# Kernel optimization log

Hardware: AMD Instinct MI355X
Metric: run time of the kernel (lower is better)

Reference implementation:

```python
import jax, jax.numpy as jnp
import numpy as np

D_MODEL = 256
NHEAD = 8
HEAD_DIM = D_MODEL // NHEAD
NUM_BOND_TYPES = 5
SCALE = float(np.sqrt(HEAD_DIM))


def setup_inputs() -> dict:
    key = jax.random.key(0)
    ks = jax.random.split(key, 12)
    B, N = 8, 1024
    s = 1.0 / np.sqrt(D_MODEL)
    x = jax.random.normal(ks[0], (B, N, D_MODEL), dtype=jnp.float32)
    adj_matrix = jax.random.randint(ks[1], (B, N, N), 0, NUM_BOND_TYPES, dtype=jnp.int32)
    Wq = jax.random.uniform(ks[2], (D_MODEL, D_MODEL), jnp.float32, -s, s)
    bq = jax.random.uniform(ks[3], (D_MODEL,), jnp.float32, -s, s)
    Wk = jax.random.uniform(ks[4], (D_MODEL, D_MODEL), jnp.float32, -s, s)
    bk = jax.random.uniform(ks[5], (D_MODEL,), jnp.float32, -s, s)
    Wv = jax.random.uniform(ks[6], (D_MODEL, D_MODEL), jnp.float32, -s, s)
    bv = jax.random.uniform(ks[7], (D_MODEL,), jnp.float32, -s, s)
    Wo = jax.random.uniform(ks[8], (D_MODEL, D_MODEL), jnp.float32, -s, s)
    bo = jax.random.uniform(ks[9], (D_MODEL,), jnp.float32, -s, s)
    # edge bias table (num_bond_types, nhead); torch init is zeros, use small randn so it matters
    edge_emb = 0.02 * jax.random.normal(ks[10], (NUM_BOND_TYPES, NHEAD), dtype=jnp.float32)
    return {"x": x, "adj_matrix": adj_matrix, "Wq": Wq, "bq": bq, "Wk": Wk, "bk": bk,
            "Wv": Wv, "bv": bv, "Wo": Wo, "bo": bo, "edge_emb": edge_emb}


def reference(x, adj_matrix, Wq, bq, Wk, bk, Wv, bv, Wo, bo, edge_emb):
    B, N, _ = x.shape
    # projections -> (B, H, N, Dh)
    def proj(W, b):
        return (x @ W.T + b).reshape(B, N, NHEAD, HEAD_DIM).transpose(0, 2, 1, 3)
    Q = proj(Wq, bq)
    K = proj(Wk, bk)
    V = proj(Wv, bv)
    scores = jnp.einsum('bhqd,bhkd->bhqk', Q, K) / SCALE  # (B,H,N,N)
    bias = edge_emb[adj_matrix]                            # (B,N,N,H)
    scores = scores + bias.transpose(0, 3, 1, 2)
    attn = jax.nn.softmax(scores, axis=-1)                 # dropout p=0 (eval) -> identity
    out = jnp.einsum('bhqk,bhkd->bhqd', attn, V)
    out = out.transpose(0, 2, 1, 3).reshape(B, N, D_MODEL)
    return out @ Wo.T + bo
```

## Files before the change

### kernel.cpp

```cpp
#include <hip/hip_runtime.h>
#include <hip/hip_bf16.h>

typedef float f32x4 __attribute__((ext_vector_type(4)));
typedef float f32x16 __attribute__((ext_vector_type(16)));
typedef __bf16 bf16x8 __attribute__((ext_vector_type(8)));
typedef unsigned int uint2v __attribute__((ext_vector_type(2)));

#define MFMA16(a, b, c) __builtin_amdgcn_mfma_f32_16x16x32_bf16((a), (b), (c), 0, 0, 0)
#define MFMA32(a, b, c) __builtin_amdgcn_mfma_f32_32x32x16_bf16((a), (b), (c), 0, 0, 0)

static __device__ __forceinline__ short f2s(float f) {
    __hip_bfloat16 h = __float2bfloat16(f);
    return *reinterpret_cast<short*>(&h);
}
static __device__ __forceinline__ unsigned int cvtpk(float lo, float hi) {
    unsigned int r;
    asm("v_cvt_pk_bf16_f32 %0, %1, %2" : "=v"(r) : "v"(lo), "v"(hi));
    return r;
}
static __device__ __forceinline__ float exp2f_fast(float x) {
#if __has_builtin(__builtin_amdgcn_exp2f)
    return __builtin_amdgcn_exp2f(x);
#else
    return exp2f(x);
#endif
}

__global__ __launch_bounds__(256)
void qkv3_and_gather(const float* __restrict__ x,
                     const float* __restrict__ Wq, const float* __restrict__ bq,
                     const float* __restrict__ Wk, const float* __restrict__ bk,
                     const float* __restrict__ Wv, const float* __restrict__ bv,
                     short* __restrict__ Qb, short* __restrict__ Kb, short* __restrict__ Vb,
                     const int* __restrict__ adj, unsigned int* __restrict__ adjG)
{
    __shared__ short As[128 * 72];
    __shared__ short Bs[3][64 * 72];

    const int bx = blockIdx.x;
    const int tid = threadIdx.x;

    if (bx < 256) {
        const int lane = tid & 63;
        const int wid = tid >> 6;
        const int wr = wid >> 1, wc = wid & 1;
        const int g = lane >> 4, li = lane & 15;

        const int m0 = (bx & 63) * 128;
        const int wc0 = (bx >> 6) * 64;

        const float* Wm[3]  = { Wq, Wk, Wv };
        const float* bm[3]  = { bq, bk, bv };
        short*       Om[3]  = { Qb, Kb, Vb };

        f32x4 acc[3][4][2] = {};

        const int sr = tid >> 4;
        const int sc4 = (tid & 15) * 4;

        for (int k0 = 0; k0 < 256; k0 += 64) {
            __syncthreads();
#pragma unroll
            for (int it = 0; it < 8; ++it) {
                int row = sr + it * 16;
                float4 v = *reinterpret_cast<const float4*>(&x[(m0 + row) * 256 + k0 + sc4]);
                short4 s4;
                s4.x = f2s(v.x); s4.y = f2s(v.y); s4.z = f2s(v.z); s4.w = f2s(v.w);
                *reinterpret_cast<short4*>(&As[row * 72 + sc4]) = s4;
            }
#pragma unroll
            for (int mat = 0; mat < 3; ++mat) {
#pragma unroll
                for (int it = 0; it < 4; ++it) {
                    int row = sr + it * 16;
                    float4 v = *reinterpret_cast<const float4*>(
                        &Wm[mat][(wc0 + row) * 256 + k0 + sc4]);
                    short4 s4;
                    s4.x = f2s(v.x); s4.y = f2s(v.y); s4.z = f2s(v.z); s4.w = f2s(v.w);
                    *reinterpret_cast<short4*>(&Bs[mat][row * 72 + sc4]) = s4;
                }
            }
            __syncthreads();
#pragma unroll
            for (int ks = 0; ks < 2; ++ks) {
                const int kb = ks * 32 + g * 8;
                bf16x8 a[4];
#pragma unroll
                for (int i = 0; i < 4; ++i)
                    a[i] = *reinterpret_cast<const bf16x8*>(&As[(wr * 64 + i * 16 + li) * 72 + kb]);
#pragma unroll
                for (int mat = 0; mat < 3; ++mat) {
                    bf16x8 bfr[2];
#pragma unroll
                    for (int j = 0; j < 2; ++j)
                        bfr[j] = *reinterpret_cast<const bf16x8*>(
                            &Bs[mat][(wc * 32 + j * 16 + li) * 72 + kb]);
#pragma unroll
                    for (int i = 0; i < 4; ++i)
#pragma unroll
                        for (int j = 0; j < 2; ++j)
                            acc[mat][i][j] = MFMA16(a[i], bfr[j], acc[mat][i][j]);
                }
            }
        }

#pragma unroll
        for (int mat = 0; mat < 3; ++mat) {
#pragma unroll
            for (int j = 0; j < 2; ++j) {
                const int colW = wc0 + wc * 32 + j * 16 + li;
                const int h = colW >> 5, d = colW & 31;
                const float bv_ = bm[mat][colW];
#pragma unroll
                for (int i = 0; i < 4; ++i) {
#pragma unroll
                    for (int r = 0; r < 4; ++r) {
                        const int row = m0 + wr * 64 + i * 16 + g * 4 + r;
                        const int bb = row >> 10, nq = row & 1023;
                        Om[mat][((bb * 8 + h) * 1024 + nq) * 32 + d] =
                            f2s(acc[mat][i][j][r] + bv_);
                    }
                }
            }
        }
    } else {
        const int gx = bx - 256;
        const int qt = gx & 31;
        const int b  = (gx >> 5) & 7;
        const int j0 = (gx >> 8) * 8;

        const int4* base = reinterpret_cast<const int4*>(
            adj + ((size_t)(b * 1024 + qt * 32)) * 1024);
        unsigned int* outT = adjG + ((size_t)(b * 32 + qt)) * 16 * 512;

        const int t = tid >> 4;
        const int i = (tid >> 1) & 7;
        const int laneb = 32 * (tid & 1);

#pragma unroll
        for (int jj = 0; jj < 8; ++jj) {
            const int j = j0 + jj;
            const int4 c = base[j * 256 + tid];
            const unsigned int packed =
                (unsigned)c.x | ((unsigned)c.y << 8) | ((unsigned)c.z << 16) | ((unsigned)c.w << 24);
            outT[t * 512 + i * 64 + (j + laneb)] = packed;
        }
    }
}

__global__ __launch_bounds__(256, 4)
void attn12(const short* __restrict__ Qb, const short* __restrict__ Kb,
            const short* __restrict__ Vb, const unsigned int* __restrict__ adjG,
            const float* __restrict__ edge_emb, short* __restrict__ AO)
{
    __shared__ __align__(16) short Ks[4][64 * 36];
    __shared__ __align__(16) short Vt[4][32 * 72];
    __shared__ float Etab[8];

    const int tid = threadIdx.x, lane = tid & 63, wid = tid >> 6;
    const int l5 = lane & 31, h32 = lane >> 5;
    const int qw = wid & 1, kh = wid >> 1;

    const int orig = blockIdx.x + blockIdx.y * 16;
    const int flat = (orig & 7) * 128 + (orig >> 3);
    const int qb = flat & 15, bh = flat >> 4;
    const int b = bh >> 3, h = bh & 7;
    const int qt = qb * 2 + qw;
    const int q  = qt * 32 + l5;

    const short* Qh = Qb + bh * (1024 * 32);
    const short* Kh = Kb + bh * (1024 * 32);
    const short* Vh = Vb + bh * (1024 * 32);
    const unsigned int* adjT = adjG + ((size_t)(b * 32 + qt)) * 16 * 512;

    if (tid < 5) Etab[tid] = __expf(edge_emb[tid * 8 + h]);

    const bf16x8 qf0 = *reinterpret_cast<const bf16x8*>(&Qh[q * 32 + h32 * 8]);
    const bf16x8 qf1 = *reinterpret_cast<const bf16x8*>(&Qh[q * 32 + 16 + h32 * 8]);

    const float c1 = 0.25503486f;
    const f32x16 zero16 = {};

    f32x16 o = {};
    float lr = 0.f;

    const int sr = tid >> 2;
    const int sc = (tid & 3) * 8;
    const int srh = sr >> 3, srl = sr & 7;
    const int scg2 = (sc >> 3) << 1;

#pragma unroll
    for (int u = 0; u < 2; ++u) {
        const int row = u * 512 + sr;
        int4 kr = *reinterpret_cast<const int4*>(&Kh[row * 32 + sc]);
        int4 vr = *reinterpret_cast<const int4*>(&Vh[row * 32 + sc]);
        short* kd = &Ks[u][sr * 36 + sc];
        *reinterpret_cast<short4*>(kd)     = *reinterpret_cast<short4*>(&kr);
        *reinterpret_cast<short4*>(kd + 4) = *(reinterpret_cast<short4*>(&kr) + 1);
        const short* vs = reinterpret_cast<const short*>(&vr);
#pragma unroll
        for (int i = 0; i < 8; ++i) {
            const int swz = srh ^ i ^ scg2;
            Vt[u][(sc + i) * 72 + swz * 8 + srl] = vs[i];
        }
    }
    __syncthreads();

    for (int t = 0; t < 8; ++t) {
        const int cur = (t & 1) * 2;
        const int tt = kh * 8 + t;

        unsigned int a4[8];
#pragma unroll
        for (int i = 0; i < 8; ++i)
            a4[i] = adjT[tt * 512 + i * 64 + lane];

        int4 kn[2], vn[2];
        if (t < 7) {
#pragma unroll
            for (int u = 0; u < 2; ++u) {
                const int row = u * 512 + (t + 1) * 64 + sr;
                kn[u] = *reinterpret_cast<const int4*>(&Kh[row * 32 + sc]);
                vn[u] = *reinterpret_cast<const int4*>(&Vh[row * 32 + sc]);
            }
        }

        f32x16 s[2];
        {
            const short* KsC = &Ks[cur + kh][0];
#pragma unroll
            for (int ks = 0; ks < 2; ++ks) {
                union { short4 h4[2]; bf16x8 v; } kfa, kfb;
                const int rowb = (ks * 32 + l5) * 36;
                kfa.h4[0] = *reinterpret_cast<const short4*>(&KsC[rowb + h32 * 8]);
                kfa.h4[1] = *reinterpret_cast<const short4*>(&KsC[rowb + h32 * 8 + 4]);
                kfb.h4[0] = *reinterpret_cast<const short4*>(&KsC[rowb + 16 + h32 * 8]);
                kfb.h4[1] = *reinterpret_cast<const short4*>(&KsC[rowb + 16 + h32 * 8 + 4]);
                s[ks] = MFMA32(kfa.v, qf0, zero16);
                s[ks] = MFMA32(kfb.v, qf1, s[ks]);
            }
        }

        unsigned int pw[2][8];
#pragma unroll
        for (int ks = 0; ks < 2; ++ks) {
#pragma unroll
            for (int rg = 0; rg < 4; ++rg) {
                const unsigned int aw4 = a4[ks * 4 + rg] << 2;
                float pv[4];
#pragma unroll
                for (int j = 0; j < 4; ++j) {
                    const float Ev = *reinterpret_cast<const float*>(
                        reinterpret_cast<const char*>(&Etab[0]) +
                        ((aw4 >> (8 * j)) & 0x3FCu));
                    const float pe = exp2f_fast(s[ks][rg * 4 + j] * c1);
                    const float pp = pe * Ev;
                    pv[j] = pp;
                    lr += pp;
                }
                pw[ks][rg * 2 + 0] = cvtpk(pv[0], pv[1]);
                pw[ks][rg * 2 + 1] = cvtpk(pv[2], pv[3]);
            }
        }

#pragma unroll
        for (int kc = 0; kc < 4; ++kc) {
            const int ks = kc >> 1, half = kc & 1;
            const unsigned int A0 = pw[ks][4 * half + 0], A1 = pw[ks][4 * half + 1];
            const unsigned int B0 = pw[ks][4 * half + 2], B1 = pw[ks][4 * half + 3];
            union { unsigned int u[4]; bf16x8 v; } P;
#if __has_builtin(__builtin_amdgcn_permlane32_swap)
            uint2v r02 = __builtin_amdgcn_permlane32_swap(A0, B0, false, false);
            uint2v r13 = __builtin_amdgcn_permlane32_swap(A1, B1, false, false);
            P.u[0] = r02.x; P.u[1] = r13.x;
            P.u[2] = r02.y; P.u[3] = r13.y;
#else
            const unsigned int send0 = h32 ? A0 : B0, send1 = h32 ? A1 : B1;
            const unsigned int rv0 = __shfl_xor(send0, 32);
            const unsigned int rv1 = __shfl_xor(send1, 32);
            const unsigned int own0 = h32 ? B0 : A0, own1 = h32 ? B1 : A1;
            P.u[0] = h32 ? rv0 : own0;
            P.u[1] = h32 ? rv1 : own1;
            P.u[2] = h32 ? own0 : rv0;
            P.u[3] = h32 ? own1 : rv1;
#endif
            const int swzr = (kc * 2 + h32) ^ (l5 & 7) ^ ((l5 >> 3) << 1);
            bf16x8 vf = *reinterpret_cast<const bf16x8*>(
                &Vt[cur + kh][l5 * 72 + swzr * 8]);
            o = MFMA32(vf, P.v, o);
        }

        if (t < 7) {
#pragma unroll
            for (int u = 0; u < 2; ++u) {
                short* kd = &Ks[(cur ^ 2) + u][sr * 36 + sc];
                *reinterpret_cast<short4*>(kd)     = *reinterpret_cast<short4*>(&kn[u]);
                *reinterpret_cast<short4*>(kd + 4) = *(reinterpret_cast<short4*>(&kn[u]) + 1);
                const short* vs = reinterpret_cast<const short*>(&vn[u]);
#pragma unroll
                for (int i = 0; i < 8; ++i) {
                    const int swz = srh ^ i ^ scg2;
                    Vt[(cur ^ 2) + u][(sc + i) * 72 + swz * 8 + srl] = vs[i];
                }
            }
            __syncthreads();
        }
    }

    float* scr = reinterpret_cast<float*>(&Ks[0][0]);
    if (kh == 1) {
        float* myb = scr + qw * 1152 + lane * 18;
        myb[0] = lr;
#pragma unroll
        for (int r = 0; r < 16; ++r) myb[1 + r] = o[r];
    }
    __syncthreads();

    if (kh == 0) {
        const float* pb = scr + qw * 1152 + lane * 18;
        float lsum = lr + pb[0];
        lsum += __shfl_xor(lsum, 32);
        const float inv = 1.0f / lsum;
        short* dst = &AO[((size_t)(b * 1024 + q)) * 256 + h * 32];
#pragma unroll
        for (int rg = 0; rg < 4; ++rg) {
            short4 s4;
            s4.x = f2s((o[rg * 4 + 0] + pb[1 + rg * 4 + 0]) * inv);
            s4.y = f2s((o[rg * 4 + 1] + pb[1 + rg * 4 + 1]) * inv);
            s4.z = f2s((o[rg * 4 + 2] + pb[1 + rg * 4 + 2]) * inv);
            s4.w = f2s((o[rg * 4 + 3] + pb[1 + rg * 4 + 3]) * inv);
            *reinterpret_cast<short4*>(&dst[rg * 8 + h32 * 4]) = s4;
        }
    }
}

__global__ __launch_bounds__(256)
void out_gemm(const short* __restrict__ AO, const float* __restrict__ Wo,
              const float* __restrict__ bo, float* __restrict__ out)
{
    __shared__ short As[128 * 72];
    __shared__ short Bs[64 * 72];

    const int tid = threadIdx.x, lane = tid & 63, wid = tid >> 6;
    const int wr = wid >> 1, wcn = wid & 1;
    const int g = lane >> 4, li = lane & 15;
    const int m0 = blockIdx.x * 128, n0 = blockIdx.y * 64;

    f32x4 acc[4][2] = {};
    const int ar = tid >> 3, ac8 = (tid & 7) * 8;
    const int br = tid >> 4, bc4 = (tid & 15) * 4;

    for (int k0 = 0; k0 < 256; k0 += 64) {
        __syncthreads();
#pragma unroll
        for (int it = 0; it < 4; ++it) {
            int row = ar + it * 32;
            *reinterpret_cast<int4*>(&As[row * 72 + ac8]) =
                *reinterpret_cast<const int4*>(&AO[(m0 + row) * 256 + k0 + ac8]);
        }
#pragma unroll
        for (int it = 0; it < 4; ++it) {
            int row = br + it * 16;
            float4 v = *reinterpret_cast<const float4*>(&Wo[(n0 + row) * 256 + k0 + bc4]);
            short4 s4; s4.x = f2s(v.x); s4.y = f2s(v.y); s4.z = f2s(v.z); s4.w = f2s(v.w);
            *reinterpret_cast<short4*>(&Bs[row * 72 + bc4]) = s4;
        }
        __syncthreads();
#pragma unroll
        for (int ks = 0; ks < 2; ++ks) {
            const int kb = ks * 32 + g * 8;
            bf16x8 a[4], bb[2];
#pragma unroll
            for (int i = 0; i < 4; ++i)
                a[i] = *reinterpret_cast<const bf16x8*>(&As[(wr * 64 + i * 16 + li) * 72 + kb]);
#pragma unroll
            for (int j = 0; j < 2; ++j)
                bb[j] = *reinterpret_cast<const bf16x8*>(&Bs[(wcn * 32 + j * 16 + li) * 72 + kb]);
#pragma unroll
            for (int i = 0; i < 4; ++i)
#pragma unroll
                for (int j = 0; j < 2; ++j)
                    acc[i][j] = MFMA16(a[i], bb[j], acc[i][j]);
        }
    }
#pragma unroll
    for (int j = 0; j < 2; ++j) {
        const int col = n0 + wcn * 32 + j * 16 + li;
        const float bv_ = bo[col];
#pragma unroll
        for (int i = 0; i < 4; ++i)
#pragma unroll
            for (int r = 0; r < 4; ++r) {
                const int row = m0 + wr * 64 + i * 16 + g * 4 + r;
                out[row * 256 + col] = acc[i][j][r] + bv_;
            }
    }
}

extern "C" void kernel_launch(void* const* d_in, const int* in_sizes, int n_in,
                              void* d_out, int out_size, void* d_ws, size_t ws_size,
                              hipStream_t stream)
{
    const float* x  = (const float*)d_in[0];
    const int*   adj = (const int*)d_in[1];
    const float* Wq = (const float*)d_in[2];
    const float* bq = (const float*)d_in[3];
    const float* Wk = (const float*)d_in[4];
    const float* bk = (const float*)d_in[5];
    const float* Wv = (const float*)d_in[6];
    const float* bv = (const float*)d_in[7];
    const float* Wo = (const float*)d_in[8];
    const float* bo = (const float*)d_in[9];
    const float* ee = (const float*)d_in[10];
    float* out = (float*)d_out;

    short* Qb = (short*)d_ws;
    short* Kb = Qb + 2 * 1024 * 1024;
    short* Vb = Kb + 2 * 1024 * 1024;
    short* AO = Vb + 2 * 1024 * 1024;
    unsigned int* adjG = (unsigned int*)(AO + 2 * 1024 * 1024);

    qkv3_and_gather<<<1280, 256, 0, stream>>>(x, Wq, bq, Wk, bk, Wv, bv,
                                              Qb, Kb, Vb, adj, adjG);
    attn12<<<dim3(16, 64), 256, 0, stream>>>(Qb, Kb, Vb, adjG, ee, AO);
    out_gemm<<<dim3(64, 4), 256, 0, stream>>>(AO, Wo, bo, out);
}
```

Measured before the change: 52.63 us.

## Fold softmax scale into Q projection and retile output GEMM to 32 columns

The softmax scale constant (log2e/sqrt(d)) is now applied to Q when the projection writes it out, which removes a multiply per score in the attention inner loop, and the row-sum accumulation is reorganised as a pairwise add. The output GEMM uses 128x32 tiles with each wave owning 32 rows, which doubles the grid to 512 blocks for better CU occupancy on a small GEMM. Scaling Q before the bf16 rounding slightly changes numerics, and the smaller tiles reload the A tile twice as often.

```diff
diff --git a/kernel.cpp b/kernel.cpp
--- a/kernel.cpp
+++ b/kernel.cpp
@@ -106,6 +106,7 @@
 
 #pragma unroll
         for (int mat = 0; mat < 3; ++mat) {
+            const float qscale = (mat == 0) ? 0.25503486f : 1.0f;
 #pragma unroll
             for (int j = 0; j < 2; ++j) {
                 const int colW = wc0 + wc * 32 + j * 16 + li;
@@ -118,7 +119,7 @@
                         const int row = m0 + wr * 64 + i * 16 + g * 4 + r;
                         const int bb = row >> 10, nq = row & 1023;
                         Om[mat][((bb * 8 + h) * 1024 + nq) * 32 + d] =
-                            f2s(acc[mat][i][j][r] + bv_);
+                            f2s((acc[mat][i][j][r] + bv_) * qscale);
                     }
                 }
             }
@@ -178,7 +179,6 @@
     const bf16x8 qf0 = *reinterpret_cast<const bf16x8*>(&Qh[q * 32 + h32 * 8]);
     const bf16x8 qf1 = *reinterpret_cast<const bf16x8*>(&Qh[q * 32 + 16 + h32 * 8]);
 
-    const float c1 = 0.25503486f;
     const f32x16 zero16 = {};
 
     f32x16 o = {};
@@ -253,11 +253,10 @@
                     const float Ev = *reinterpret_cast<const float*>(
                         reinterpret_cast<const char*>(&Etab[0]) +
                         ((aw4 >> (8 * j)) & 0x3FCu));
-                    const float pe = exp2f_fast(s[ks][rg * 4 + j] * c1);
-                    const float pp = pe * Ev;
-                    pv[j] = pp;
-                    lr += pp;
+                    const float pe = exp2f_fast(s[ks][rg * 4 + j]);
+                    pv[j] = pe * Ev;
                 }
+                lr += (pv[0] + pv[1]) + (pv[2] + pv[3]);
                 pw[ks][rg * 2 + 0] = cvtpk(pv[0], pv[1]);
                 pw[ks][rg * 2 + 1] = cvtpk(pv[2], pv[3]);
             }
@@ -335,20 +334,19 @@
 }
 
 __global__ __launch_bounds__(256)
-void out_gemm(const short* __restrict__ AO, const float* __restrict__ Wo,
-              const float* __restrict__ bo, float* __restrict__ out)
+void out_gemm32(const short* __restrict__ AO, const float* __restrict__ Wo,
+                const float* __restrict__ bo, float* __restrict__ out)
 {
     __shared__ short As[128 * 72];
-    __shared__ short Bs[64 * 72];
+    __shared__ short Bs[32 * 72];
 
     const int tid = threadIdx.x, lane = tid & 63, wid = tid >> 6;
-    const int wr = wid >> 1, wcn = wid & 1;
     const int g = lane >> 4, li = lane & 15;
-    const int m0 = blockIdx.x * 128, n0 = blockIdx.y * 64;
-
-    f32x4 acc[4][2] = {};
+    const int m0 = blockIdx.x * 128, n0 = blockIdx.y * 32;
+
+    f32x4 acc[2][2] = {};
     const int ar = tid >> 3, ac8 = (tid & 7) * 8;
-    const int br = tid >> 4, bc4 = (tid & 15) * 4;
+    const int br = tid >> 3, bc8 = (tid & 7) * 8;
 
     for (int k0 = 0; k0 < 256; k0 += 64) {
         __syncthreads();
@@ -358,26 +356,28 @@
             *reinterpret_cast<int4*>(&As[row * 72 + ac8]) =
                 *reinterpret_cast<const int4*>(&AO[(m0 + row) * 256 + k0 + ac8]);
         }
-#pragma unroll
-        for (int it = 0; it < 4; ++it) {
-            int row = br + it * 16;
-            float4 v = *reinterpret_cast<const float4*>(&Wo[(n0 + row) * 256 + k0 + bc4]);
-            short4 s4; s4.x = f2s(v.x); s4.y = f2s(v.y); s4.z = f2s(v.z); s4.w = f2s(v.w);
-            *reinterpret_cast<short4*>(&Bs[row * 72 + bc4]) = s4;
+        {
+            float4 v0 = *reinterpret_cast<const float4*>(&Wo[(n0 + br) * 256 + k0 + bc8]);
+            float4 v1 = *reinterpret_cast<const float4*>(&Wo[(n0 + br) * 256 + k0 + bc8 + 4]);
+            short4 s0, s1;
+            s0.x = f2s(v0.x); s0.y = f2s(v0.y); s0.z = f2s(v0.z); s0.w = f2s(v0.w);
+            s1.x = f2s(v1.x); s1.y = f2s(v1.y); s1.z = f2s(v1.z); s1.w = f2s(v1.w);
+            *reinterpret_cast<short4*>(&Bs[br * 72 + bc8])     = s0;
+            *reinterpret_cast<short4*>(&Bs[br * 72 + bc8 + 4]) = s1;
         }
         __syncthreads();
 #pragma unroll
         for (int ks = 0; ks < 2; ++ks) {
             const int kb = ks * 32 + g * 8;
-            bf16x8 a[4], bb[2];
-#pragma unroll
-            for (int i = 0; i < 4; ++i)
-                a[i] = *reinterpret_cast<const bf16x8*>(&As[(wr * 64 + i * 16 + li) * 72 + kb]);
+            bf16x8 a[2], bb[2];
+#pragma unroll
+            for (int i = 0; i < 2; ++i)
+                a[i] = *reinterpret_cast<const bf16x8*>(&As[(wid * 32 + i * 16 + li) * 72 + kb]);
 #pragma unroll
             for (int j = 0; j < 2; ++j)
-                bb[j] = *reinterpret_cast<const bf16x8*>(&Bs[(wcn * 32 + j * 16 + li) * 72 + kb]);
-#pragma unroll
-            for (int i = 0; i < 4; ++i)
+                bb[j] = *reinterpret_cast<const bf16x8*>(&Bs[(j * 16 + li) * 72 + kb]);
+#pragma unroll
+            for (int i = 0; i < 2; ++i)
 #pragma unroll
                 for (int j = 0; j < 2; ++j)
                     acc[i][j] = MFMA16(a[i], bb[j], acc[i][j]);
@@ -385,13 +385,13 @@
     }
 #pragma unroll
     for (int j = 0; j < 2; ++j) {
-        const int col = n0 + wcn * 32 + j * 16 + li;
+        const int col = n0 + j * 16 + li;
         const float bv_ = bo[col];
 #pragma unroll
-        for (int i = 0; i < 4; ++i)
+        for (int i = 0; i < 2; ++i)
 #pragma unroll
             for (int r = 0; r < 4; ++r) {
-                const int row = m0 + wr * 64 + i * 16 + g * 4 + r;
+                const int row = m0 + wid * 32 + i * 16 + g * 4 + r;
                 out[row * 256 + col] = acc[i][j][r] + bv_;
             }
     }
@@ -423,5 +423,5 @@
     qkv3_and_gather<<<1280, 256, 0, stream>>>(x, Wq, bq, Wk, bk, Wv, bv,
                                               Qb, Kb, Vb, adj, adjG);
     attn12<<<dim3(16, 64), 256, 0, stream>>>(Qb, Kb, Vb, adjG, ee, AO);
-    out_gemm<<<dim3(64, 4), 256, 0, stream>>>(AO, Wo, bo, out);
-}
+    out_gemm32<<<dim3(64, 8), 256, 0, stream>>>(AO, Wo, bo, out);
+}
```

New measurement: 51.25 us. -2.6%, faster.
